# Performance work log

Measured on AMD Instinct MI355X. Metric: run time of the kernel, lower is better.

## Reference

```python
import jax, jax.numpy as jnp
import numpy as np

FP8 = jnp.float8_e4m3fn  # HPU fp8_143 format used by fp8_gemm_v2


def setup_inputs() -> dict:
    key = jax.random.key(0)
    k1, k2 = jax.random.split(key)
    B, S, K, N = 16, 4096, 128, 4096
    x = jax.random.normal(k1, (B, S, K), dtype=jnp.float32)
    y = jax.random.normal(k2, (K, N), dtype=jnp.float32)
    x_scale = jnp.ones((1,), dtype=jnp.float32)
    y_scale = jnp.ones((1,), dtype=jnp.float32)
    return {"x": x, "y": y, "x_scale": x_scale, "y_scale": y_scale}


def reference(x, y, x_scale, y_scale):
    # QuantizedModule.forward: qx = cast_to_fp8(x * scale)
    qx = (x * x_scale).astype(FP8)
    qy = (y * y_scale).astype(FP8)
    # fp8_gemm_v2(qx, qy, out_dtype=x.dtype, inv_x_scale, inv_y_scale):
    # GEMM on fp8 operands with inline dequant by 1/x_scale and 1/y_scale.
    out = jnp.matmul(qx.astype(jnp.float32), qy.astype(jnp.float32))
    inv_scale = (1.0 / x_scale) * (1.0 / y_scale)  # scalar (shape [1])
    return out * inv_scale[0]
```

## Files before the change

### kernel.cpp

```cpp
#include <hip/hip_runtime.h>

typedef __attribute__((ext_vector_type(16))) float f32x16;
typedef unsigned long long u64;

__global__ void quant_pack_all(const float* __restrict__ x,
                               const float* __restrict__ y,
                               const float* __restrict__ xs,
                               const float* __restrict__ ys,
                               u64* __restrict__ ap, u64* __restrict__ bp,
                               int N, int tx, int total) {
    int t = blockIdx.x * blockDim.x + threadIdx.x;
    if (t >= total) return;
    if (t < tx) {
        float s = xs[0];
        int lane = t & 63;
        int kk   = (t >> 6) & 7;
        int m32  = t >> 9;
        int r = lane & 31, h = lane >> 5;
        const float* src = x + ((size_t)(m32 * 32 + r)) * 128 + kk * 16 + h * 8;
        float4 a = *reinterpret_cast<const float4*>(src);
        float4 b = *reinterpret_cast<const float4*>(src + 4);
        int lo = 0, hi = 0;
        lo = __builtin_amdgcn_cvt_pk_fp8_f32(a.x * s, a.y * s, lo, false);
        lo = __builtin_amdgcn_cvt_pk_fp8_f32(a.z * s, a.w * s, lo, true);
        hi = __builtin_amdgcn_cvt_pk_fp8_f32(b.x * s, b.y * s, hi, false);
        hi = __builtin_amdgcn_cvt_pk_fp8_f32(b.z * s, b.w * s, hi, true);
        ap[t] = ((u64)(unsigned int)hi << 32) | (unsigned int)lo;
    } else {
        t -= tx;
        float s = ys[0];
        int lane = t & 63;
        int kk   = (t >> 6) & 7;
        int n32  = t >> 9;
        int c = lane & 31, h = lane >> 5;
        const float* src = y + (size_t)(kk * 16 + h * 8) * N + n32 * 32 + c;
        float v[8];
#pragma unroll
        for (int j = 0; j < 8; ++j) v[j] = src[(size_t)j * N] * s;
        int lo = 0, hi = 0;
        lo = __builtin_amdgcn_cvt_pk_fp8_f32(v[0], v[1], lo, false);
        lo = __builtin_amdgcn_cvt_pk_fp8_f32(v[2], v[3], lo, true);
        hi = __builtin_amdgcn_cvt_pk_fp8_f32(v[4], v[5], hi, false);
        hi = __builtin_amdgcn_cvt_pk_fp8_f32(v[6], v[7], hi, true);
        bp[t] = ((u64)(unsigned int)hi << 32) | (unsigned int)lo;
    }
}

__global__ __launch_bounds__(256) void gemm_fp8_kernel(
    const u64* __restrict__ ap, const u64* __restrict__ bp,
    const float* __restrict__ xs, const float* __restrict__ ys,
    float* __restrict__ out, int M, int N, int nb) {
    int nwg = gridDim.x;
    int cpx = nwg >> 3;
    int bid = blockIdx.x;
    int swz = (bid & 7) * cpx + (bid >> 3);
    int bx  = swz % nb;
    int by  = swz / nb;

    int wid  = threadIdx.x >> 6;
    int lane = threadIdx.x & 63;
    int m0   = by * 32;
    int n0   = bx * 512 + wid * 128;

    float inv = 1.0f / (xs[0] * ys[0]);

    const u64* abase = ap + (size_t)(m0 >> 5) * 512 + lane;
    const u64* bbase = bp + (size_t)(n0 >> 5) * 512 + lane;

    f32x16 acc[4] = {};

#pragma unroll
    for (int kk = 0; kk < 8; ++kk) {
        long a = (long)abase[kk * 64];
#pragma unroll
        for (int nf = 0; nf < 4; ++nf) {
            long b = (long)bbase[(size_t)nf * 512 + kk * 64];
            acc[nf] = __builtin_amdgcn_mfma_f32_32x32x16_fp8_fp8(a, b, acc[nf], 0, 0, 0);
        }
    }

    int col = lane & 31;
    int h4  = (lane >> 5) * 4;
#pragma unroll
    for (int rg = 0; rg < 16; ++rg) {
        int row = (rg & 3) + 8 * (rg >> 2) + h4;
        float* o = out + (size_t)(m0 + row) * N + n0 + col;
#pragma unroll
        for (int nf = 0; nf < 4; ++nf)
            __builtin_nontemporal_store(acc[nf][rg] * inv, o + nf * 32);
    }
}

extern "C" void kernel_launch(void* const* d_in, const int* in_sizes, int n_in,
                              void* d_out, int out_size, void* d_ws, size_t ws_size,
                              hipStream_t stream) {
    const float* x  = (const float*)d_in[0];
    const float* y  = (const float*)d_in[1];
    const float* xs = (const float*)d_in[2];
    const float* ys = (const float*)d_in[3];
    float* out = (float*)d_out;

    const int K = 128;
    int M = in_sizes[0] / K;
    int N = in_sizes[1] / K;

    u64* ap = (u64*)d_ws;
    u64* bp = ap + (size_t)M * K / 8;

    int tx = M * (K / 8);
    int ty = N * (K / 8);
    int total = tx + ty;
    quant_pack_all<<<(total + 255) / 256, 256, 0, stream>>>(x, y, xs, ys, ap, bp,
                                                            N, tx, total);

    int nb = N / 512;
    int grid = (M / 32) * nb;
    gemm_fp8_kernel<<<grid, 256, 0, stream>>>(ap, bp, xs, ys, out, M, N, nb);
}
```

Before: 189.3 us.

## Fuse x quantization into GEMM kernel, drop packed A workspace

Stops pre-quantizing x into a packed fp8 workspace. The GEMM kernel now loads fp32 rows of x directly, scales them and converts to fp8 fragments in registers, and only y is quantized in a separate pass. This removes a 32 MB fp32 read plus an 8 MB fp8 write and read round trip through global memory. The cost is that x is reread as fp32 by every block sharing an M tile (N/512 = 8 column blocks), and the quantization work is repeated per wave.

```diff
diff --git a/kernel.cpp b/kernel.cpp
--- a/kernel.cpp
+++ b/kernel.cpp
@@ -3,51 +3,30 @@
 typedef __attribute__((ext_vector_type(16))) float f32x16;
 typedef unsigned long long u64;
 
-__global__ void quant_pack_all(const float* __restrict__ x,
-                               const float* __restrict__ y,
-                               const float* __restrict__ xs,
-                               const float* __restrict__ ys,
-                               u64* __restrict__ ap, u64* __restrict__ bp,
-                               int N, int tx, int total) {
+__global__ void quant_y_pack(const float* __restrict__ y,
+                             const float* __restrict__ scale,
+                             u64* __restrict__ bp, int N, int total) {
     int t = blockIdx.x * blockDim.x + threadIdx.x;
     if (t >= total) return;
-    if (t < tx) {
-        float s = xs[0];
-        int lane = t & 63;
-        int kk   = (t >> 6) & 7;
-        int m32  = t >> 9;
-        int r = lane & 31, h = lane >> 5;
-        const float* src = x + ((size_t)(m32 * 32 + r)) * 128 + kk * 16 + h * 8;
-        float4 a = *reinterpret_cast<const float4*>(src);
-        float4 b = *reinterpret_cast<const float4*>(src + 4);
-        int lo = 0, hi = 0;
-        lo = __builtin_amdgcn_cvt_pk_fp8_f32(a.x * s, a.y * s, lo, false);
-        lo = __builtin_amdgcn_cvt_pk_fp8_f32(a.z * s, a.w * s, lo, true);
-        hi = __builtin_amdgcn_cvt_pk_fp8_f32(b.x * s, b.y * s, hi, false);
-        hi = __builtin_amdgcn_cvt_pk_fp8_f32(b.z * s, b.w * s, hi, true);
-        ap[t] = ((u64)(unsigned int)hi << 32) | (unsigned int)lo;
-    } else {
-        t -= tx;
-        float s = ys[0];
-        int lane = t & 63;
-        int kk   = (t >> 6) & 7;
-        int n32  = t >> 9;
-        int c = lane & 31, h = lane >> 5;
-        const float* src = y + (size_t)(kk * 16 + h * 8) * N + n32 * 32 + c;
-        float v[8];
+    float s = scale[0];
+    int lane = t & 63;
+    int kk   = (t >> 6) & 7;
+    int n32  = t >> 9;
+    int c = lane & 31, h = lane >> 5;
+    const float* src = y + (size_t)(kk * 16 + h * 8) * N + n32 * 32 + c;
+    float v[8];
 #pragma unroll
-        for (int j = 0; j < 8; ++j) v[j] = src[(size_t)j * N] * s;
-        int lo = 0, hi = 0;
-        lo = __builtin_amdgcn_cvt_pk_fp8_f32(v[0], v[1], lo, false);
-        lo = __builtin_amdgcn_cvt_pk_fp8_f32(v[2], v[3], lo, true);
-        hi = __builtin_amdgcn_cvt_pk_fp8_f32(v[4], v[5], hi, false);
-        hi = __builtin_amdgcn_cvt_pk_fp8_f32(v[6], v[7], hi, true);
-        bp[t] = ((u64)(unsigned int)hi << 32) | (unsigned int)lo;
-    }
+    for (int j = 0; j < 8; ++j) v[j] = src[(size_t)j * N] * s;
+    int lo = 0, hi = 0;
+    lo = __builtin_amdgcn_cvt_pk_fp8_f32(v[0], v[1], lo, false);
+    lo = __builtin_amdgcn_cvt_pk_fp8_f32(v[2], v[3], lo, true);
+    hi = __builtin_amdgcn_cvt_pk_fp8_f32(v[4], v[5], hi, false);
+    hi = __builtin_amdgcn_cvt_pk_fp8_f32(v[6], v[7], hi, true);
+    bp[t] = ((u64)(unsigned int)hi << 32) | (unsigned int)lo;
 }
 
 __global__ __launch_bounds__(256) void gemm_fp8_kernel(
-    const u64* __restrict__ ap, const u64* __restrict__ bp,
+    const float* __restrict__ x, const u64* __restrict__ bp,
     const float* __restrict__ xs, const float* __restrict__ ys,
     float* __restrict__ out, int M, int N, int nb) {
     int nwg = gridDim.x;
@@ -59,19 +38,35 @@
 
     int wid  = threadIdx.x >> 6;
     int lane = threadIdx.x & 63;
+    int r    = lane & 31;
+    int h    = lane >> 5;
     int m0   = by * 32;
     int n0   = bx * 512 + wid * 128;
 
+    float s   = xs[0];
     float inv = 1.0f / (xs[0] * ys[0]);
 
-    const u64* abase = ap + (size_t)(m0 >> 5) * 512 + lane;
+    const float* xsrc = x + (size_t)(m0 + r) * 128 + h * 8;
+    u64 afr[8];
+#pragma unroll
+    for (int kk = 0; kk < 8; ++kk) {
+        float4 a = *reinterpret_cast<const float4*>(xsrc + kk * 16);
+        float4 b = *reinterpret_cast<const float4*>(xsrc + kk * 16 + 4);
+        int lo = 0, hi = 0;
+        lo = __builtin_amdgcn_cvt_pk_fp8_f32(a.x * s, a.y * s, lo, false);
+        lo = __builtin_amdgcn_cvt_pk_fp8_f32(a.z * s, a.w * s, lo, true);
+        hi = __builtin_amdgcn_cvt_pk_fp8_f32(b.x * s, b.y * s, hi, false);
+        hi = __builtin_amdgcn_cvt_pk_fp8_f32(b.z * s, b.w * s, hi, true);
+        afr[kk] = ((u64)(unsigned int)hi << 32) | (unsigned int)lo;
+    }
+
     const u64* bbase = bp + (size_t)(n0 >> 5) * 512 + lane;
 
     f32x16 acc[4] = {};
 
 #pragma unroll
     for (int kk = 0; kk < 8; ++kk) {
-        long a = (long)abase[kk * 64];
+        long a = (long)afr[kk];
 #pragma unroll
         for (int nf = 0; nf < 4; ++nf) {
             long b = (long)bbase[(size_t)nf * 512 + kk * 64];
@@ -80,7 +75,7 @@
     }
 
     int col = lane & 31;
-    int h4  = (lane >> 5) * 4;
+    int h4  = h * 4;
 #pragma unroll
     for (int rg = 0; rg < 16; ++rg) {
         int row = (rg & 3) + 8 * (rg >> 2) + h4;
@@ -104,16 +99,12 @@
     int M = in_sizes[0] / K;
     int N = in_sizes[1] / K;
 
-    u64* ap = (u64*)d_ws;
-    u64* bp = ap + (size_t)M * K / 8;
+    u64* bp = (u64*)d_ws;
 
-    int tx = M * (K / 8);
     int ty = N * (K / 8);
-    int total = tx + ty;
-    quant_pack_all<<<(total + 255) / 256, 256, 0, stream>>>(x, y, xs, ys, ap, bp,
-                                                            N, tx, total);
+    quant_y_pack<<<(ty + 255) / 256, 256, 0, stream>>>(y, ys, bp, N, ty);
 
     int nb = N / 512;
     int grid = (M / 32) * nb;
-    gemm_fp8_kernel<<<grid, 256, 0, stream>>>(ap, bp, xs, ys, out, M, N, nb);
+    gemm_fp8_kernel<<<grid, 256, 0, stream>>>(x, bp, xs, ys, out, M, N, nb);
 }
```

Result: slower. 224.3 us (+18.5%).
